# Performance work log

Measured on AMD Instinct MI355X. Metric: run time of the kernel, lower is better.

The kernel has to match this reference:

```python
import jax, jax.numpy as jnp
from jax import lax
import numpy as np

DN = ('NCHW', 'OIHW', 'NCHW')

def conv(x, w, b, stride=1, groups=1):
    y = lax.conv_general_dilated(x, w, (stride, stride), 'SAME',
                                 feature_group_count=groups, dimension_numbers=DN)
    return y + b[None, :, None, None]

def sep_conv(x, dw, pw, pb):
    # depthwise 3x3 -> pointwise 1x1 -> ReLU (BN is frozen at identity)
    y = lax.conv_general_dilated(x, dw, (1, 1), 'SAME',
                                 feature_group_count=x.shape[1], dimension_numbers=DN)
    return jax.nn.relu(conv(y, pw, pb))

def up2(x):
    return jnp.repeat(jnp.repeat(x, 2, axis=2), 2, axis=3)

def down2(x):
    return lax.reduce_window(x, -jnp.inf, lax.max, (1, 1, 2, 2), (1, 1, 2, 2), 'VALID')

def fuse(w, *xs):
    # fast normalized fusion
    w = jax.nn.relu(w)
    w = w / (jnp.sum(w) + 1e-4)
    out = w[0] * xs[0]
    for i in range(1, len(xs)):
        out = out + w[i] * xs[i]
    return out

def bifpn_layer(ps, dw, pw, pb, fw2, fw3):
    p3, p4, p5, p6, p7 = ps
    p6t = sep_conv(fuse(fw2[0], p6, up2(p7)),  dw[0], pw[0], pb[0])
    p5t = sep_conv(fuse(fw2[1], p5, up2(p6t)), dw[1], pw[1], pb[1])
    p4t = sep_conv(fuse(fw2[2], p4, up2(p5t)), dw[2], pw[2], pb[2])
    p3o = sep_conv(fuse(fw2[3], p3, up2(p4t)), dw[3], pw[3], pb[3])
    p4o = sep_conv(fuse(fw3[0], p4, p4t, down2(p3o)), dw[4], pw[4], pb[4])
    p5o = sep_conv(fuse(fw3[1], p5, p5t, down2(p4o)), dw[5], pw[5], pb[5])
    p6o = sep_conv(fuse(fw3[2], p6, p6t, down2(p5o)), dw[6], pw[6], pb[6])
    p7o = sep_conv(fuse(fw2[4], p7, down2(p6o)),      dw[7], pw[7], pb[7])
    return [p3o, p4o, p5o, p6o, p7o]

def make_anchors(img_size):
    # RetinaNet-style anchors: pyramid levels 3..7, 3 scales x 3 ratios
    ratios = np.array([0.5, 1.0, 2.0])
    scales = 2.0 ** (np.arange(3) / 3.0)
    boxes_all = []
    for lvl in range(3, 8):
        stride = 2 ** lvl
        size = 2 ** (lvl + 2)
        fs = img_size // stride
        ws = (size * scales[None, :] / np.sqrt(ratios)[:, None]).reshape(-1)  # [9]
        hs = (size * scales[None, :] * np.sqrt(ratios)[:, None]).reshape(-1)
        ctr = (np.arange(fs) + 0.5) * stride
        gy, gx = np.meshgrid(ctr, ctr, indexing='ij')
        centers = np.stack([gx, gy], -1).reshape(-1, 1, 2)      # [HW,1,2] (x,y)
        wh = np.stack([ws, hs], -1)[None]                       # [1,9,2]
        boxes = np.concatenate([centers - wh / 2, centers + wh / 2], -1).reshape(-1, 4)
        boxes_all.append(boxes)
    return jnp.asarray(np.concatenate(boxes_all, 0), jnp.float32)

def run_head(p, tw, tb, ow, ob, out_ch):
    x = p
    for i in range(tw.shape[0]):
        x = jax.nn.relu(conv(x, tw[i], tb[i]))
    y = conv(x, ow, ob)                                  # [B, 9*out_ch, H, W]
    B, _, H, W = y.shape
    return y.transpose(0, 2, 3, 1).reshape(B, H * W * 9, out_ch)

def setup_inputs() -> dict:
    key = jax.random.key(0)
    ks = iter(jax.random.split(key, 64))
    B, W, NC, ST, D = 4, 88, 90, 3, 4
    chans = [40, 80, 112, 192, 320]
    hw = [64, 32, 16, 8, 4]
    inp = {}
    for i, (c, h) in enumerate(zip(chans, hw)):
        inp[f'c{i+3}'] = jax.random.normal(next(ks), (B, c, h, h), jnp.float32)
        inp[f'lat_w{i+3}'] = jax.random.normal(next(ks), (W, c, 1, 1), jnp.float32) * 0.05
        inp[f'lat_b{i+3}'] = jnp.zeros((W,), jnp.float32)
    inp['bif_dw'] = jax.random.normal(next(ks), (ST, 8, W, 1, 3, 3), jnp.float32) * 0.1
    inp['bif_pw'] = jax.random.normal(next(ks), (ST, 8, W, W, 1, 1), jnp.float32) * 0.05
    inp['bif_pb'] = jnp.zeros((ST, 8, W), jnp.float32)
    inp['bif_fw2'] = jnp.ones((ST, 5, 2), jnp.float32)
    inp['bif_fw3'] = jnp.ones((ST, 3, 3), jnp.float32)
    inp['reg_tw'] = jax.random.normal(next(ks), (D, W, W, 3, 3), jnp.float32) * 0.03
    inp['reg_tb'] = jnp.zeros((D, W), jnp.float32)
    inp['reg_ow'] = jax.random.normal(next(ks), (36, W, 3, 3), jnp.float32) * 0.01
    inp['reg_ob'] = jnp.zeros((36,), jnp.float32)
    inp['cls_tw'] = jax.random.normal(next(ks), (D, W, W, 3, 3), jnp.float32) * 0.03
    inp['cls_tb'] = jnp.zeros((D, W), jnp.float32)
    inp['cls_ow'] = jax.random.normal(next(ks), (9 * NC, W, 3, 3), jnp.float32) * 0.01
    inp['cls_ob'] = jnp.full((9 * NC,), -np.log((1.0 - 0.01) / 0.01), jnp.float32)
    inp['img_size'] = 512
    return inp

def reference(c3, c4, c5, c6, c7,
              lat_w3, lat_b3, lat_w4, lat_b4, lat_w5, lat_b5,
              lat_w6, lat_b6, lat_w7, lat_b7,
              bif_dw, bif_pw, bif_pb, bif_fw2, bif_fw3,
              reg_tw, reg_tb, reg_ow, reg_ob,
              cls_tw, cls_tb, cls_ow, cls_ob,
              img_size):
    num_classes = cls_ow.shape[0] // 9
    ps = [conv(c3, lat_w3, lat_b3), conv(c4, lat_w4, lat_b4), conv(c5, lat_w5, lat_b5),
          conv(c6, lat_w6, lat_b6), conv(c7, lat_w7, lat_b7)]
    for s in range(bif_dw.shape[0]):
        ps = bifpn_layer(ps, bif_dw[s], bif_pw[s], bif_pb[s], bif_fw2[s], bif_fw3[s])
    regression = jnp.concatenate([run_head(p, reg_tw, reg_tb, reg_ow, reg_ob, 4) for p in ps], axis=1)
    classification = jnp.concatenate(
        [jax.nn.sigmoid(run_head(p, cls_tw, cls_tb, cls_ow, cls_ob, num_classes)) for p in ps], axis=1)
    anchors = make_anchors(int(img_size))
    return classification, regression, anchors
```

## Files before the change

kernel.cpp:

```cpp
#include <hip/hip_runtime.h>
#include <math.h>

#define TPB 256
static inline int cdiv(int a, int b) { return (a + b - 1) / b; }

typedef __attribute__((ext_vector_type(8))) short short8;
typedef __attribute__((ext_vector_type(4))) float floatx4;

__device__ __forceinline__ float bf2f(ushort u) {
    union { unsigned int u; float f; } v; v.u = ((unsigned int)u) << 16; return v.f;
}
__device__ __forceinline__ ushort f2bf(float f) {
    union { float f; unsigned int u; } v; v.f = f;
    unsigned int r = (v.u + 0x7FFFu + ((v.u >> 16) & 1u)) >> 16;
    return (ushort)r;
}

#define CONC_ROWS 21824
__device__ __forceinline__ void lvl_of(int row, int& lvl, int& base) {
    lvl = 0; base = 0;
    if (row >= 16384) { lvl = 1; base = 16384; }
    if (row >= 20480) { lvl = 2; base = 20480; }
    if (row >= 21504) { lvl = 3; base = 21504; }
    if (row >= 21760) { lvl = 4; base = 21760; }
}
__constant__ int LOFFc[5] = {0, 36864, 46080, 48384, 48960};

__global__ void pack3_k(const float* __restrict__ w, ushort* __restrict__ Bp,
                        int Ntot, int CO, int total) {
    int idx = blockIdx.x * blockDim.x + threadIdx.x;
    if (idx >= total) return;
    int j = idx & 7; int t = idx >> 3;
    int n = t % Ntot; t /= Ntot;
    int g = t & 3; t >>= 2;
    int ks = t % 3; int tap = t / 3;
    int ci = ks * 32 + g * 8 + j;
    float v = (ci < 88 && n < CO) ? w[((size_t)n * 88 + ci) * 9 + tap] : 0.f;
    Bp[idx] = f2bf(v);
}

__global__ void pack_tw8_k(const float* __restrict__ rw, const float* __restrict__ cw,
                           ushort* __restrict__ Bp) {
    int idx = blockIdx.x * blockDim.x + threadIdx.x;
    if (idx >= 8 * 82944) return;
    int i = idx / 82944; int r = idx - i * 82944;
    const float* w = (i < 4) ? rw + (size_t)i * 69696 : cw + (size_t)(i - 4) * 69696;
    int j = r & 7; int t = r >> 3;
    int n = t % 96; t /= 96;
    int g = t & 3; t >>= 2;
    int ks = t % 3; int tap = t / 3;
    int ci = ks * 32 + g * 8 + j;
    float v = (ci < 88 && n < 88) ? w[((size_t)n * 88 + ci) * 9 + tap] : 0.f;
    Bp[idx] = f2bf(v);
}

__global__ void pack_pw_all_k(const float* __restrict__ pw, ushort* __restrict__ Bp,
                              int total) {
    int idx = blockIdx.x * blockDim.x + threadIdx.x;
    if (idx >= total) return;
    int cid = idx / 9216; int r = idx - cid * 9216;
    int j = r & 7; int t = r >> 3;
    int n = t % 96; t /= 96;
    int g = t & 3; int ks = t >> 2;
    int ci = ks * 32 + g * 8 + j;
    float v = (ci < 88 && n < 88) ? pw[(size_t)cid * 7744 + n * 88 + ci] : 0.f;
    Bp[idx] = f2bf(v);
}

__global__ void pack_lat_k(const float* __restrict__ w3, const float* __restrict__ w4,
                           const float* __restrict__ w5, const float* __restrict__ w6,
                           const float* __restrict__ w7, ushort* __restrict__ Bp) {
    int idx = blockIdx.x * blockDim.x + threadIdx.x;
    if (idx >= 76800) return;
    int l, off;
    if (idx < 6144)       { l = 0; off = 0; }
    else if (idx < 15360) { l = 1; off = 6144; }
    else if (idx < 27648) { l = 2; off = 15360; }
    else if (idx < 46080) { l = 3; off = 27648; }
    else                  { l = 4; off = 46080; }
    const float* w = l == 0 ? w3 : l == 1 ? w4 : l == 2 ? w5 : l == 3 ? w6 : w7;
    const int cins[5] = {40, 80, 112, 192, 320};
    int Cin = cins[l];
    int r = idx - off;
    int j = r & 7; int t = r >> 3;
    int n = t % 96; t /= 96;
    int g = t & 3; int ks = t >> 2;
    int ci = ks * 32 + g * 8 + j;
    float v = (ci < Cin && n < 88) ? w[(size_t)n * Cin + ci] : 0.f;
    Bp[idx] = f2bf(v);
}

__global__ __launch_bounds__(256)
void lateral_mfma_k(const float* __restrict__ x, const ushort* __restrict__ Bp,
                    const float* __restrict__ bias, ushort* __restrict__ out,
                    int Cin, int KS, int logHH) {
    __shared__ ushort As[64 * 40];
    int tid = threadIdx.x;
    int m0 = blockIdx.x * 64;
    int lane = tid & 63, l15 = lane & 15, g = (lane >> 4) & 3;
    int wave = tid >> 6, wm = wave & 1, wn = wave >> 1;
    floatx4 acc[2][3];
#pragma unroll
    for (int a = 0; a < 2; ++a)
#pragma unroll
        for (int b = 0; b < 3; ++b) acc[a][b] = (floatx4){0.f, 0.f, 0.f, 0.f};
    const short8* Bq = (const short8*)Bp;

    int p = m0 + lane;
    int n = p >> logHH, pp = p & ((1 << logHH) - 1);
    const float* xp = x + (((size_t)n * Cin) << logHH) + pp;

    for (int ks = 0; ks < KS; ++ks) {
        __syncthreads();
#pragma unroll
        for (int it = 0; it < 8; ++it) {
            int ciL = (tid >> 6) + it * 4;
            int ci = ks * 32 + ciL;
            float v = (ci < Cin) ? xp[(size_t)ci << logHH] : 0.f;
            As[lane * 40 + ciL] = f2bf(v);
        }
        __syncthreads();
        short8 a0 = *(const short8*)(&As[(wm * 32 + l15) * 40 + g * 8]);
        short8 a1 = *(const short8*)(&As[(wm * 32 + 16 + l15) * 40 + g * 8]);
        int bbase = (ks * 4 + g) * 96 + wn * 48 + l15;
#pragma unroll
        for (int nf = 0; nf < 3; ++nf) {
            short8 b = Bq[bbase + nf * 16];
            acc[0][nf] = __builtin_amdgcn_mfma_f32_16x16x32_bf16(a0, b, acc[0][nf], 0, 0, 0);
            acc[1][nf] = __builtin_amdgcn_mfma_f32_16x16x32_bf16(a1, b, acc[1][nf], 0, 0, 0);
        }
    }
    float bc[3];
#pragma unroll
    for (int nf = 0; nf < 3; ++nf) {
        int c = wn * 48 + nf * 16 + l15;
        bc[nf] = (c < 88) ? bias[c] : 0.f;
    }
#pragma unroll
    for (int mf = 0; mf < 2; ++mf)
#pragma unroll
        for (int r = 0; r < 4; ++r) {
            int pl = m0 + wm * 32 + mf * 16 + g * 4 + r;
#pragma unroll
            for (int nf = 0; nf < 3; ++nf) {
                int c = wn * 48 + nf * 16 + l15;
                out[(size_t)pl * 96 + c] = f2bf(acc[mf][nf][r] + bc[nf]);
            }
        }
}

template <int MODE>
__global__ void fusedw_k(const ushort* __restrict__ a, const ushort* __restrict__ b,
                         const ushort* __restrict__ cmap, const float* __restrict__ fw,
                         const float* __restrict__ dww, ushort* __restrict__ out,
                         int logH, int total) {
    int idx = blockIdx.x * blockDim.x + threadIdx.x;
    if (idx >= total) return;
    int c = idx % 96, p = idx / 96;
    if (c >= 88) { out[idx] = 0; return; }
    int H = 1 << logH;
    int HH = H * H;
    int n = p >> (2 * logH), pp = p & (HH - 1);
    int y = pp >> logH, x = pp & (H - 1);
    float w0 = fmaxf(fw[0], 0.f), w1 = fmaxf(fw[1], 0.f);
    float w2 = (MODE == 2) ? fmaxf(fw[2], 0.f) : 0.f;
    float inv = 1.f / (w0 + w1 + w2 + 1e-4f);
    const float* wp = dww + c * 9;
    float acc = 0.f;
#pragma unroll
    for (int ky = 0; ky < 3; ++ky) {
        int sy = y + ky - 1;
        if (sy < 0 || sy >= H) continue;
#pragma unroll
        for (int kx = 0; kx < 3; ++kx) {
            int sx = x + kx - 1;
            if (sx < 0 || sx >= H) continue;
            int np = n * HH + sy * H + sx;
            float av = bf2f(a[(size_t)np * 96 + c]);
            float fv;
            if (MODE == 0) {
                int Hh = H >> 1;
                int bp = n * Hh * Hh + (sy >> 1) * Hh + (sx >> 1);
                fv = (w0 * av + w1 * bf2f(b[(size_t)bp * 96 + c])) * inv;
            } else {
                int H2 = H * 2;
                const ushort* q = (MODE == 1 ? b : cmap) +
                    ((size_t)(n * H2 * H2 + 2 * sy * H2 + 2 * sx)) * 96 + c;
                float m = fmaxf(fmaxf(bf2f(q[0]), bf2f(q[96])),
                                fmaxf(bf2f(q[H2 * 96]), bf2f(q[H2 * 96 + 96])));
                if (MODE == 1) fv = (w0 * av + w1 * m) * inv;
                else {
                    float b2v = bf2f(b[(size_t)np * 96 + c]);
                    fv = (w0 * av + w1 * b2v + w2 * m) * inv;
                }
            }
            acc = fmaf(fv, wp[ky * 3 + kx], acc);
        }
    }
    out[idx] = f2bf(acc);
}

__global__ __launch_bounds__(256)
void pw_mfma_k(const ushort* __restrict__ in, const ushort* __restrict__ Bp,
               const float* __restrict__ bias, ushort* __restrict__ out) {
    __shared__ ushort As[64 * 104];
    int tid = threadIdx.x;
    int m0 = blockIdx.x * 64;
    int lane = tid & 63, l15 = lane & 15, g = (lane >> 4) & 3;
    int wave = tid >> 6, wm = wave & 1, wn = wave >> 1;
    floatx4 acc[2][3];
#pragma unroll
    for (int a = 0; a < 2; ++a)
#pragma unroll
        for (int b = 0; b < 3; ++b) acc[a][b] = (floatx4){0.f, 0.f, 0.f, 0.f};
    const short8* Bq = (const short8*)Bp;
#pragma unroll
    for (int it = 0; it < 3; ++it) {
        int cc = tid + it * 256;
        int row = cc / 12, cg = cc - row * 12;
        *(uint4*)(&As[row * 104 + cg * 8]) =
            *(const uint4*)(in + (size_t)(m0 + row) * 96 + cg * 8);
    }
    __syncthreads();
#pragma unroll
    for (int ks = 0; ks < 3; ++ks) {
        int k = ks * 32 + g * 8;
        short8 a0 = *(const short8*)(&As[(wm * 32 + l15) * 104 + k]);
        short8 a1 = *(const short8*)(&As[(wm * 32 + 16 + l15) * 104 + k]);
        int bbase = (ks * 4 + g) * 96 + wn * 48 + l15;
#pragma unroll
        for (int nf = 0; nf < 3; ++nf) {
            short8 b = Bq[bbase + nf * 16];
            acc[0][nf] = __builtin_amdgcn_mfma_f32_16x16x32_bf16(a0, b, acc[0][nf], 0, 0, 0);
            acc[1][nf] = __builtin_amdgcn_mfma_f32_16x16x32_bf16(a1, b, acc[1][nf], 0, 0, 0);
        }
    }
    float bc[3];
#pragma unroll
    for (int nf = 0; nf < 3; ++nf) {
        int c = wn * 48 + nf * 16 + l15;
        bc[nf] = (c < 88) ? bias[c] : 0.f;
    }
#pragma unroll
    for (int mf = 0; mf < 2; ++mf)
#pragma unroll
        for (int r = 0; r < 4; ++r) {
            int pl = m0 + wm * 32 + mf * 16 + g * 4 + r;
#pragma unroll
            for (int nf = 0; nf < 3; ++nf) {
                int c = wn * 48 + nf * 16 + l15;
                out[(size_t)pl * 96 + c] = f2bf(fmaxf(acc[mf][nf][r] + bc[nf], 0.f));
            }
        }
}

__global__ __launch_bounds__(256)
void tower_mfma_k(const ushort* __restrict__ inR, const ushort* __restrict__ inC,
                  const ushort* __restrict__ BpR, const ushort* __restrict__ BpC,
                  const float* __restrict__ bR, const float* __restrict__ bC,
                  ushort* __restrict__ outR, ushort* __restrict__ outC) {
    int head = blockIdx.y;
    const ushort* in = head ? inC : inR;
    const ushort* Bp = head ? BpC : BpR;
    const float* bias = head ? bC : bR;
    ushort* out = head ? outC : outR;

    __shared__ ushort As[64 * 104];
    int tid = threadIdx.x;
    int m0 = blockIdx.x * 64;
    int lvl, base; lvl_of(m0, lvl, base);
    int logW = 6 - lvl, W = 1 << logW, HH = W * W, log2HH = 2 * logW;
    int pl0 = m0 - base;
    int lane = tid & 63, l15 = lane & 15, g = (lane >> 4) & 3;
    int wave = tid >> 6, wm = wave & 1, wn = wave >> 1;
    floatx4 acc[2][3];
#pragma unroll
    for (int a = 0; a < 2; ++a)
#pragma unroll
        for (int b = 0; b < 3; ++b) acc[a][b] = (floatx4){0.f, 0.f, 0.f, 0.f};
    const short8* Bq = (const short8*)Bp;

#pragma unroll
    for (int tap = 0; tap < 9; ++tap) {
        int dy = tap / 3 - 1, dx = tap % 3 - 1;
        __syncthreads();
#pragma unroll
        for (int it = 0; it < 3; ++it) {
            int cc = tid + it * 256;
            int row = cc / 12, cg = cc - row * 12;
            int pl = pl0 + row;
            int n = pl >> log2HH, pp = pl & (HH - 1);
            int y = pp >> logW, x = pp & (W - 1);
            int sy = y + dy, sx = x + dx;
            uint4 v = {0u, 0u, 0u, 0u};
            if (sy >= 0 && sy < W && sx >= 0 && sx < W)
                v = *(const uint4*)(in + ((size_t)(base + (n << log2HH) + (sy << logW) + sx)) * 96 + cg * 8);
            *(uint4*)(&As[row * 104 + cg * 8]) = v;
        }
        __syncthreads();
#pragma unroll
        for (int ks = 0; ks < 3; ++ks) {
            int k = ks * 32 + g * 8;
            short8 a0 = *(const short8*)(&As[(wm * 32 + l15) * 104 + k]);
            short8 a1 = *(const short8*)(&As[(wm * 32 + 16 + l15) * 104 + k]);
            int bbase = ((tap * 3 + ks) * 4 + g) * 96 + wn * 48 + l15;
#pragma unroll
            for (int nf = 0; nf < 3; ++nf) {
                short8 b = Bq[bbase + nf * 16];
                acc[0][nf] = __builtin_amdgcn_mfma_f32_16x16x32_bf16(a0, b, acc[0][nf], 0, 0, 0);
                acc[1][nf] = __builtin_amdgcn_mfma_f32_16x16x32_bf16(a1, b, acc[1][nf], 0, 0, 0);
            }
        }
    }
    float bc[3];
#pragma unroll
    for (int nf = 0; nf < 3; ++nf) {
        int c = wn * 48 + nf * 16 + l15;
        bc[nf] = (c < 88) ? bias[c] : 0.f;
    }
#pragma unroll
    for (int mf = 0; mf < 2; ++mf)
#pragma unroll
        for (int r = 0; r < 4; ++r) {
            int pl = m0 + wm * 32 + mf * 16 + g * 4 + r;
#pragma unroll
            for (int nf = 0; nf < 3; ++nf) {
                int c = wn * 48 + nf * 16 + l15;
                out[(size_t)pl * 96 + c] = f2bf(fmaxf(acc[mf][nf][r] + bc[nf], 0.f));
            }
        }
}

template <bool SIG>
__global__ __launch_bounds__(256)
void head_out_all_k(const ushort* __restrict__ in, const ushort* __restrict__ Bp,
                    const float* __restrict__ bias, float* __restrict__ outb,
                    int Ntot, int C9, int OC) {
    __shared__ ushort As[64 * 104];
    int tid = threadIdx.x;
    int m0 = blockIdx.x * 64;
    int n0b = blockIdx.y * 96;
    int lvl, base; lvl_of(m0, lvl, base);
    int logW = 6 - lvl, W = 1 << logW, HH = W * W, log2HH = 2 * logW;
    int pl0 = m0 - base;
    int lane = tid & 63, l15 = lane & 15, g = (lane >> 4) & 3;
    int wave = tid >> 6, wm = wave & 1, wn = wave >> 1;
    floatx4 acc[2][3];
#pragma unroll
    for (int a = 0; a < 2; ++a)
#pragma unroll
        for (int b = 0; b < 3; ++b) acc[a][b] = (floatx4){0.f, 0.f, 0.f, 0.f};
    const short8* Bq = (const short8*)Bp;

    for (int tap = 0; tap < 9; ++tap) {
        int dy = tap / 3 - 1, dx = tap % 3 - 1;
        __syncthreads();
#pragma unroll
        for (int it = 0; it < 3; ++it) {
            int cc = tid + it * 256;
            int row = cc / 12, cg = cc - row * 12;
            int pl = pl0 + row;
            int n = pl >> log2HH, pp = pl & (HH - 1);
            int y = pp >> logW, x = pp & (W - 1);
            int sy = y + dy, sx = x + dx;
            uint4 v = {0u, 0u, 0u, 0u};
            if (sy >= 0 && sy < W && sx >= 0 && sx < W)
                v = *(const uint4*)(in + ((size_t)(base + (n << log2HH) + (sy << logW) + sx)) * 96 + cg * 8);
            *(uint4*)(&As[row * 104 + cg * 8]) = v;
        }
        __syncthreads();
#pragma unroll
        for (int ks = 0; ks < 3; ++ks) {
            int k = ks * 32 + g * 8;
            short8 a0 = *(const short8*)(&As[(wm * 32 + l15) * 104 + k]);
            short8 a1 = *(const short8*)(&As[(wm * 32 + 16 + l15) * 104 + k]);
            int bbase = ((tap * 3 + ks) * 4 + g) * Ntot + n0b + wn * 48 + l15;
#pragma unroll
            for (int nf = 0; nf < 3; ++nf) {
                short8 b = Bq[bbase + nf * 16];
                acc[0][nf] = __builtin_amdgcn_mfma_f32_16x16x32_bf16(a0, b, acc[0][nf], 0, 0, 0);
                acc[1][nf] = __builtin_amdgcn_mfma_f32_16x16x32_bf16(a1, b, acc[1][nf], 0, 0, 0);
            }
        }
    }
#pragma unroll
    for (int nf = 0; nf < 3; ++nf) {
        int c = n0b + wn * 48 + nf * 16 + l15;
        if (c >= C9) continue;
        float bcv = bias[c];
        int a = c / OC, kk = c - a * OC;
#pragma unroll
        for (int mf = 0; mf < 2; ++mf)
#pragma unroll
            for (int r = 0; r < 4; ++r) {
                int pl = pl0 + wm * 32 + mf * 16 + g * 4 + r;
                int n = pl >> log2HH, pp = pl & (HH - 1);
                float v = acc[mf][nf][r] + bcv;
                if (SIG) v = 1.f / (1.f + expf(-v));
                outb[((size_t)n * 49104 + LOFFc[lvl] + (size_t)pp * 9 + a) * OC + kk] = v;
            }
    }
}

__global__ void anchors_k(float* __restrict__ out) {
    int idx = blockIdx.x * blockDim.x + threadIdx.x;
    if (idx >= 49104) return;
    const int offs[6] = {0, 36864, 46080, 48384, 48960, 49104};
    int l = 0;
    while (idx >= offs[l + 1]) ++l;
    int j = idx - offs[l];
    int a = j % 9;
    int p = j / 9;
    int fs = 64 >> l;
    int stride = 8 << l;
    float size = (float)(32 << l);
    int ix = p % fs, iy = p / fs;
    float cx = (ix + 0.5f) * (float)stride;
    float cy = (iy + 0.5f) * (float)stride;
    const float scl[3] = {1.0f, 1.2599210498948732f, 1.5874010519681994f};
    const float sqr[3] = {0.7071067811865476f, 1.0f, 1.4142135623730951f};
    int r = a / 3, s = a % 3;
    float w = size * scl[s] / sqr[r];
    float h = size * scl[s] * sqr[r];
    float* o = out + (size_t)idx * 4;
    o[0] = cx - 0.5f * w;
    o[1] = cy - 0.5f * h;
    o[2] = cx + 0.5f * w;
    o[3] = cy + 0.5f * h;
}


extern "C" void kernel_launch(void* const* d_in, const int* in_sizes, int n_in,
                              void* d_out, int out_size, void* d_ws, size_t ws_size,
                              hipStream_t stream) {
    const float* c_in[5]  = {(const float*)d_in[0],  (const float*)d_in[3],
                             (const float*)d_in[6],  (const float*)d_in[9],
                             (const float*)d_in[12]};
    const float* lat_w[5] = {(const float*)d_in[1],  (const float*)d_in[4],
                             (const float*)d_in[7],  (const float*)d_in[10],
                             (const float*)d_in[13]};
    const float* lat_b[5] = {(const float*)d_in[2],  (const float*)d_in[5],
                             (const float*)d_in[8],  (const float*)d_in[11],
                             (const float*)d_in[14]};
    const float* bif_dw  = (const float*)d_in[15];
    const float* bif_pw  = (const float*)d_in[16];
    const float* bif_pb  = (const float*)d_in[17];
    const float* bif_fw2 = (const float*)d_in[18];
    const float* bif_fw3 = (const float*)d_in[19];
    const float* reg_tw  = (const float*)d_in[20];
    const float* reg_tb  = (const float*)d_in[21];
    const float* reg_ow  = (const float*)d_in[22];
    const float* reg_ob  = (const float*)d_in[23];
    const float* cls_tw  = (const float*)d_in[24];
    const float* cls_tb  = (const float*)d_in[25];
    const float* cls_ow  = (const float*)d_in[26];
    const float* cls_ob  = (const float*)d_in[27];

    const int HS[5]   = {64, 32, 16, 8, 4};
    const int CINL[5] = {40, 80, 112, 192, 320};
    const int KSL[5]  = {2, 3, 4, 6, 10};
    const int LATO[5] = {0, 6144, 15360, 27648, 46080};
    const int ROFF[5] = {0, 16384, 20480, 21504, 21760};
    const int ML[5]   = {16384, 4096, 1024, 256, 64};
    const size_t CONC = (size_t)CONC_ROWS * 96;

    ushort* ws = (ushort*)d_ws;
    size_t off = 0;
    ushort* CA = ws + off; off += CONC;
    ushort* CB = ws + off; off += CONC;
    ushort* T4 = ws + off; off += (size_t)4096 * 96;
    ushort* T5 = ws + off; off += (size_t)1024 * 96;
    ushort* T6 = ws + off; off += (size_t)256 * 96;
    ushort* DT = ws + off; off += (size_t)16384 * 96;
    ushort* HXR0 = ws + off; off += CONC;
    ushort* HXR1 = ws + off; off += CONC;
    ushort* HXC0 = ws + off; off += CONC;
    ushort* HXC1 = ws + off; off += CONC;
    ushort* BP_PW  = ws + off; off += (size_t)24 * 9216;
    ushort* BP_TW  = ws + off; off += (size_t)8 * 82944;
    ushort* BP_RO  = ws + off; off += (size_t)82944;
    ushort* BP_CO  = ws + off; off += (size_t)746496;
    ushort* BP_LAT = ws + off; off += (size_t)76800;
    (void)ws_size; (void)n_in; (void)in_sizes; (void)out_size;

    pack_pw_all_k<<<cdiv(24 * 9216, TPB), TPB, 0, stream>>>(bif_pw, BP_PW, 24 * 9216);
    pack_tw8_k<<<cdiv(8 * 82944, TPB), TPB, 0, stream>>>(reg_tw, cls_tw, BP_TW);
    pack3_k<<<cdiv(82944, TPB), TPB, 0, stream>>>(reg_ow, BP_RO, 96, 36, 82944);
    pack3_k<<<cdiv(746496, TPB), TPB, 0, stream>>>(cls_ow, BP_CO, 864, 810, 746496);
    pack_lat_k<<<cdiv(76800, TPB), TPB, 0, stream>>>(
        lat_w[0], lat_w[1], lat_w[2], lat_w[3], lat_w[4], BP_LAT);

    float* cls_base = (float*)d_out;
    float* reg_base = cls_base + (size_t)4 * 49104 * 90;
    float* anc_base = reg_base + (size_t)4 * 49104 * 4;
    anchors_k<<<cdiv(49104, TPB), TPB, 0, stream>>>(anc_base);

    for (int l = 0; l < 5; ++l) {
        int logHH = 2 * (6 - l);
        lateral_mfma_k<<<ML[l] / 64, 256, 0, stream>>>(
            c_in[l], BP_LAT + LATO[l], lat_b[l], CA + (size_t)ROFF[l] * 96,
            CINL[l], KSL[l], logHH);
    }

    ushort* cur = CA; ushort* nxt = CB;
    for (int s = 0; s < 3; ++s) {
        const float* dws = bif_dw + (size_t)s * 8 * 792;
        const float* pbs = bif_pb + (size_t)s * 8 * 88;
        const float* f2  = bif_fw2 + (size_t)s * 10;
        const float* f3  = bif_fw3 + (size_t)s * 9;
        auto LP = [&](ushort* buf, int l) { return buf + (size_t)ROFF[l] * 96; };
        auto pw = [&](int ci, const ushort* src, ushort* dst, int l) {
            pw_mfma_k<<<ML[l] / 64, 256, 0, stream>>>(
                src, BP_PW + (size_t)(s * 8 + ci) * 9216, pbs + ci * 88, dst);
        };

        { int l = 3, t = ML[l] * 96;
          fusedw_k<0><<<cdiv(t, TPB), TPB, 0, stream>>>(
              LP(cur, 3), LP(cur, 4), nullptr, f2 + 0, dws + 0 * 792, DT, 6 - l, t);
          pw(0, DT, T6, l); }
        { int l = 2, t = ML[l] * 96;
          fusedw_k<0><<<cdiv(t, TPB), TPB, 0, stream>>>(
              LP(cur, 2), T6, nullptr, f2 + 2, dws + 1 * 792, DT, 6 - l, t);
          pw(1, DT, T5, l); }
        { int l = 1, t = ML[l] * 96;
          fusedw_k<0><<<cdiv(t, TPB), TPB, 0, stream>>>(
              LP(cur, 1), T5, nullptr, f2 + 4, dws + 2 * 792, DT, 6 - l, t);
          pw(2, DT, T4, l); }
        { int l = 0, t = ML[l] * 96;
          fusedw_k<0><<<cdiv(t, TPB), TPB, 0, stream>>>(
              LP(cur, 0), T4, nullptr, f2 + 6, dws + 3 * 792, DT, 6 - l, t);
          pw(3, DT, LP(nxt, 0), l); }
        { int l = 1, t = ML[l] * 96;
          fusedw_k<2><<<cdiv(t, TPB), TPB, 0, stream>>>(
              LP(cur, 1), T4, LP(nxt, 0), f3 + 0, dws + 4 * 792, DT, 6 - l, t);
          pw(4, DT, LP(nxt, 1), l); }
        { int l = 2, t = ML[l] * 96;
          fusedw_k<2><<<cdiv(t, TPB), TPB, 0, stream>>>(
              LP(cur, 2), T5, LP(nxt, 1), f3 + 3, dws + 5 * 792, DT, 6 - l, t);
          pw(5, DT, LP(nxt, 2), l); }
        { int l = 3, t = ML[l] * 96;
          fusedw_k<2><<<cdiv(t, TPB), TPB, 0, stream>>>(
              LP(cur, 3), T6, LP(nxt, 2), f3 + 6, dws + 6 * 792, DT, 6 - l, t);
          pw(6, DT, LP(nxt, 3), l); }
        { int l = 4, t = ML[l] * 96;
          fusedw_k<1><<<cdiv(t, TPB), TPB, 0, stream>>>(
              LP(cur, 4), LP(nxt, 3), nullptr, f2 + 8, dws + 7 * 792, DT, 6 - l, t);
          pw(7, DT, LP(nxt, 4), l); }

        ushort* tp = cur; cur = nxt; nxt = tp;
    }

    ushort* hxr[2] = {HXR0, HXR1};
    ushort* hxc[2] = {HXC0, HXC1};
    const ushort* xr = cur;
    const ushort* xc = cur;
    const int GB = CONC_ROWS / 64;
    for (int i = 0; i < 4; ++i) {
        tower_mfma_k<<<dim3(GB, 2), 256, 0, stream>>>(
            xr, xc, BP_TW + (size_t)i * 82944, BP_TW + (size_t)(4 + i) * 82944,
            reg_tb + i * 88, cls_tb + i * 88, hxr[i & 1], hxc[i & 1]);
        xr = hxr[i & 1]; xc = hxc[i & 1];
    }
    head_out_all_k<false><<<dim3(GB, 1), 256, 0, stream>>>(
        xr, BP_RO, reg_ob, reg_base, 96, 36, 4);
    head_out_all_k<true><<<dim3(GB, 9), 256, 0, stream>>>(
        xc, BP_CO, cls_ob, cls_base, 864, 810, 90);
}
```

Measured before the change: 686.5 us.

## Fuse BiFPN depthwise+pointwise into one kernel and use halo tiles for head convs

```diff
diff --git a/kernel.cpp b/kernel.cpp
--- a/kernel.cpp
+++ b/kernel.cpp
@@ -25,6 +25,7 @@
     if (row >= 21760) { lvl = 4; base = 21760; }
 }
 __constant__ int LOFFc[5] = {0, 36864, 46080, 48384, 48960};
+__constant__ int MLVc[5]  = {16384, 4096, 1024, 256, 64};
 
 __global__ void pack3_k(const float* __restrict__ w, ushort* __restrict__ Bp,
                         int Ntot, int CO, int total) {
@@ -150,83 +151,130 @@
 }
 
 template <int MODE>
-__global__ void fusedw_k(const ushort* __restrict__ a, const ushort* __restrict__ b,
-                         const ushort* __restrict__ cmap, const float* __restrict__ fw,
-                         const float* __restrict__ dww, ushort* __restrict__ out,
-                         int logH, int total) {
-    int idx = blockIdx.x * blockDim.x + threadIdx.x;
-    if (idx >= total) return;
-    int c = idx % 96, p = idx / 96;
-    if (c >= 88) { out[idx] = 0; return; }
-    int H = 1 << logH;
-    int HH = H * H;
-    int n = p >> (2 * logH), pp = p & (HH - 1);
-    int y = pp >> logH, x = pp & (H - 1);
+__global__ __launch_bounds__(256, 2)
+void sepconv_k(const ushort* __restrict__ a, const ushort* __restrict__ bsrc,
+               const ushort* __restrict__ csrc, const float* __restrict__ fw,
+               const float* __restrict__ dww, const ushort* __restrict__ Bp,
+               const float* __restrict__ pbias, ushort* __restrict__ out,
+               int logW) {
+    __shared__ ushort Fs[195 * 104];
+    __shared__ ushort Ds[64 * 104];
+    __shared__ ushort Dwb[108 * 8];
+    int tid = threadIdx.x;
+    int W = 1 << logW, HH = W * W, log2HH = 2 * logW;
+    int Mlv = 4 * HH;
+    int HB = W + 1;
+    int RS = 64 + 2 * HB;
+    int pl0 = blockIdx.x * 64;
     float w0 = fmaxf(fw[0], 0.f), w1 = fmaxf(fw[1], 0.f);
     float w2 = (MODE == 2) ? fmaxf(fw[2], 0.f) : 0.f;
     float inv = 1.f / (w0 + w1 + w2 + 1e-4f);
-    const float* wp = dww + c * 9;
-    float acc = 0.f;
-#pragma unroll
-    for (int ky = 0; ky < 3; ++ky) {
-        int sy = y + ky - 1;
-        if (sy < 0 || sy >= H) continue;
-#pragma unroll
-        for (int kx = 0; kx < 3; ++kx) {
-            int sx = x + kx - 1;
-            if (sx < 0 || sx >= H) continue;
-            int np = n * HH + sy * H + sx;
-            float av = bf2f(a[(size_t)np * 96 + c]);
-            float fv;
+    float w0i = w0 * inv, w1i = w1 * inv, w2i = w2 * inv;
+
+    if (tid < 13) *(uint4*)(&Fs[194 * 104 + tid * 8]) = (uint4){0u, 0u, 0u, 0u};
+    for (int i = tid; i < 108; i += 256) {
+        int cg = i / 9, tap = i - cg * 9;
+        ushort tmp[8];
+#pragma unroll
+        for (int j = 0; j < 8; ++j) {
+            int c = cg * 8 + j;
+            tmp[j] = (c < 88) ? f2bf(dww[c * 9 + tap]) : (ushort)0;
+        }
+        *(uint4*)(&Dwb[i * 8]) = *(uint4*)tmp;
+    }
+    for (int i = tid; i < RS * 12; i += 256) {
+        int row = i / 12, cg = i - row * 12;
+        int pl = pl0 - HB + row;
+        uint4 res = {0u, 0u, 0u, 0u};
+        if (pl >= 0 && pl < Mlv) {
+            int n = pl >> log2HH, pp = pl & (HH - 1);
+            int y = pp >> logW, x = pp & (W - 1);
+            uint4 av = *(const uint4*)(a + (size_t)pl * 96 + cg * 8);
+            const ushort* au = (const ushort*)&av;
+            float f[8];
             if (MODE == 0) {
-                int Hh = H >> 1;
-                int bp = n * Hh * Hh + (sy >> 1) * Hh + (sx >> 1);
-                fv = (w0 * av + w1 * bf2f(b[(size_t)bp * 96 + c])) * inv;
+                int Wh = W >> 1;
+                int bp = (n << (log2HH - 2)) + (y >> 1) * Wh + (x >> 1);
+                uint4 bv = *(const uint4*)(bsrc + (size_t)bp * 96 + cg * 8);
+                const ushort* bu = (const ushort*)&bv;
+#pragma unroll
+                for (int j = 0; j < 8; ++j)
+                    f[j] = w0i * bf2f(au[j]) + w1i * bf2f(bu[j]);
             } else {
-                int H2 = H * 2;
-                const ushort* q = (MODE == 1 ? b : cmap) +
-                    ((size_t)(n * H2 * H2 + 2 * sy * H2 + 2 * sx)) * 96 + c;
-                float m = fmaxf(fmaxf(bf2f(q[0]), bf2f(q[96])),
-                                fmaxf(bf2f(q[H2 * 96]), bf2f(q[H2 * 96 + 96])));
-                if (MODE == 1) fv = (w0 * av + w1 * m) * inv;
-                else {
-                    float b2v = bf2f(b[(size_t)np * 96 + c]);
-                    fv = (w0 * av + w1 * b2v + w2 * m) * inv;
+                int W2 = W << 1;
+                const ushort* q = (MODE == 1 ? bsrc : csrc) +
+                    ((size_t)((n << (log2HH + 2)) + (2 * y) * W2 + 2 * x)) * 96 + cg * 8;
+                uint4 q0 = *(const uint4*)(q);
+                uint4 q1 = *(const uint4*)(q + 96);
+                uint4 q2 = *(const uint4*)(q + (size_t)W2 * 96);
+                uint4 q3 = *(const uint4*)(q + (size_t)W2 * 96 + 96);
+                const ushort* u0 = (const ushort*)&q0; const ushort* u1 = (const ushort*)&q1;
+                const ushort* u2 = (const ushort*)&q2; const ushort* u3 = (const ushort*)&q3;
+                if (MODE == 1) {
+#pragma unroll
+                    for (int j = 0; j < 8; ++j) {
+                        float m = fmaxf(fmaxf(bf2f(u0[j]), bf2f(u1[j])),
+                                        fmaxf(bf2f(u2[j]), bf2f(u3[j])));
+                        f[j] = w0i * bf2f(au[j]) + w1i * m;
+                    }
+                } else {
+                    uint4 b2v = *(const uint4*)(bsrc + (size_t)pl * 96 + cg * 8);
+                    const ushort* b2u = (const ushort*)&b2v;
+#pragma unroll
+                    for (int j = 0; j < 8; ++j) {
+                        float m = fmaxf(fmaxf(bf2f(u0[j]), bf2f(u1[j])),
+                                        fmaxf(bf2f(u2[j]), bf2f(u3[j])));
+                        f[j] = w0i * bf2f(au[j]) + w1i * bf2f(b2u[j]) + w2i * m;
+                    }
                 }
             }
-            acc = fmaf(fv, wp[ky * 3 + kx], acc);
-        }
-    }
-    out[idx] = f2bf(acc);
-}
-
-__global__ __launch_bounds__(256)
-void pw_mfma_k(const ushort* __restrict__ in, const ushort* __restrict__ Bp,
-               const float* __restrict__ bias, ushort* __restrict__ out) {
-    __shared__ ushort As[64 * 104];
-    int tid = threadIdx.x;
-    int m0 = blockIdx.x * 64;
+            ushort tmp[8];
+#pragma unroll
+            for (int j = 0; j < 8; ++j) tmp[j] = f2bf(f[j]);
+            res = *(uint4*)tmp;
+        }
+        *(uint4*)(&Fs[row * 104 + cg * 8]) = res;
+    }
+    __syncthreads();
+    for (int i = tid; i < 768; i += 256) {
+        int row = i / 12, cg = i - row * 12;
+        int pl = pl0 + row;
+        int pp = pl & (HH - 1);
+        int y = pp >> logW, x = pp & (W - 1);
+        float acc8[8] = {0.f, 0.f, 0.f, 0.f, 0.f, 0.f, 0.f, 0.f};
+        if (cg < 11) {
+#pragma unroll
+            for (int tap = 0; tap < 9; ++tap) {
+                int dy = tap / 3 - 1, dx = tap % 3 - 1;
+                int sy = y + dy, sx = x + dx;
+                bool pred = ((unsigned)sy < (unsigned)W) && ((unsigned)sx < (unsigned)W);
+                int rsel = pred ? (row + HB + dy * W + dx) : 194;
+                short8 fv = *(const short8*)(&Fs[rsel * 104 + cg * 8]);
+                short8 wv = *(const short8*)(&Dwb[(cg * 9 + tap) * 8]);
+#pragma unroll
+                for (int j = 0; j < 8; ++j)
+                    acc8[j] = fmaf(bf2f((ushort)fv[j]), bf2f((ushort)wv[j]), acc8[j]);
+            }
+        }
+        ushort tmp[8];
+#pragma unroll
+        for (int j = 0; j < 8; ++j) tmp[j] = f2bf(acc8[j]);
+        *(uint4*)(&Ds[row * 104 + cg * 8]) = *(uint4*)tmp;
+    }
+    __syncthreads();
     int lane = tid & 63, l15 = lane & 15, g = (lane >> 4) & 3;
     int wave = tid >> 6, wm = wave & 1, wn = wave >> 1;
     floatx4 acc[2][3];
 #pragma unroll
-    for (int a = 0; a < 2; ++a)
-#pragma unroll
-        for (int b = 0; b < 3; ++b) acc[a][b] = (floatx4){0.f, 0.f, 0.f, 0.f};
+    for (int aa = 0; aa < 2; ++aa)
+#pragma unroll
+        for (int bb = 0; bb < 3; ++bb) acc[aa][bb] = (floatx4){0.f, 0.f, 0.f, 0.f};
     const short8* Bq = (const short8*)Bp;
-#pragma unroll
-    for (int it = 0; it < 3; ++it) {
-        int cc = tid + it * 256;
-        int row = cc / 12, cg = cc - row * 12;
-        *(uint4*)(&As[row * 104 + cg * 8]) =
-            *(const uint4*)(in + (size_t)(m0 + row) * 96 + cg * 8);
-    }
-    __syncthreads();
 #pragma unroll
     for (int ks = 0; ks < 3; ++ks) {
         int k = ks * 32 + g * 8;
-        short8 a0 = *(const short8*)(&As[(wm * 32 + l15) * 104 + k]);
-        short8 a1 = *(const short8*)(&As[(wm * 32 + 16 + l15) * 104 + k]);
+        short8 a0 = *(const short8*)(&Ds[(wm * 32 + l15) * 104 + k]);
+        short8 a1 = *(const short8*)(&Ds[(wm * 32 + 16 + l15) * 104 + k]);
         int bbase = (ks * 4 + g) * 96 + wn * 48 + l15;
 #pragma unroll
         for (int nf = 0; nf < 3; ++nf) {
@@ -239,13 +287,13 @@
 #pragma unroll
     for (int nf = 0; nf < 3; ++nf) {
         int c = wn * 48 + nf * 16 + l15;
-        bc[nf] = (c < 88) ? bias[c] : 0.f;
+        bc[nf] = (c < 88) ? pbias[c] : 0.f;
     }
 #pragma unroll
     for (int mf = 0; mf < 2; ++mf)
 #pragma unroll
         for (int r = 0; r < 4; ++r) {
-            int pl = m0 + wm * 32 + mf * 16 + g * 4 + r;
+            int pl = pl0 + wm * 32 + mf * 16 + g * 4 + r;
 #pragma unroll
             for (int nf = 0; nf < 3; ++nf) {
                 int c = wn * 48 + nf * 16 + l15;
@@ -254,61 +302,73 @@
         }
 }
 
-__global__ __launch_bounds__(256)
-void tower_mfma_k(const ushort* __restrict__ inR, const ushort* __restrict__ inC,
+__global__ __launch_bounds__(256, 2)
+void tower_halo_k(const ushort* __restrict__ inR, const ushort* __restrict__ inC,
                   const ushort* __restrict__ BpR, const ushort* __restrict__ BpC,
                   const float* __restrict__ bR, const float* __restrict__ bC,
                   ushort* __restrict__ outR, ushort* __restrict__ outC) {
+    __shared__ ushort As[259 * 104];
     int head = blockIdx.y;
     const ushort* in = head ? inC : inR;
-    const ushort* Bp = head ? BpC : BpR;
+    const short8* Bq = (const short8*)(head ? BpC : BpR);
     const float* bias = head ? bC : bR;
     ushort* out = head ? outC : outR;
-
-    __shared__ ushort As[64 * 104];
     int tid = threadIdx.x;
-    int m0 = blockIdx.x * 64;
+    int m0 = blockIdx.x * 128;
     int lvl, base; lvl_of(m0, lvl, base);
     int logW = 6 - lvl, W = 1 << logW, HH = W * W, log2HH = 2 * logW;
-    int pl0 = m0 - base;
+    int Mlv = MLVc[lvl];
+    int HB = W + 1;
+    int RS = 128 + 2 * HB;
+    if (tid < 13) *(uint4*)(&As[258 * 104 + tid * 8]) = (uint4){0u, 0u, 0u, 0u};
+    for (int i = tid; i < RS * 12; i += 256) {
+        int row = i / 12, cg = i - row * 12;
+        int pl = m0 - base - HB + row;
+        uint4 v = {0u, 0u, 0u, 0u};
+        if (pl >= 0 && pl < Mlv)
+            v = *(const uint4*)(in + (size_t)(base + pl) * 96 + cg * 8);
+        *(uint4*)(&As[row * 104 + cg * 8]) = v;
+    }
+    __syncthreads();
     int lane = tid & 63, l15 = lane & 15, g = (lane >> 4) & 3;
     int wave = tid >> 6, wm = wave & 1, wn = wave >> 1;
-    floatx4 acc[2][3];
-#pragma unroll
-    for (int a = 0; a < 2; ++a)
-#pragma unroll
-        for (int b = 0; b < 3; ++b) acc[a][b] = (floatx4){0.f, 0.f, 0.f, 0.f};
-    const short8* Bq = (const short8*)Bp;
-
+    int pl0 = m0 - base;
+    int rL[4], xm[4], ym[4]; bool vm[4];
+#pragma unroll
+    for (int mf = 0; mf < 4; ++mf) {
+        rL[mf] = wm * 64 + mf * 16 + l15;
+        int pl = pl0 + rL[mf];
+        vm[mf] = pl < Mlv;
+        int pp = pl & (HH - 1);
+        ym[mf] = pp >> logW; xm[mf] = pp & (W - 1);
+    }
+    floatx4 acc[4][3];
+#pragma unroll
+    for (int aa = 0; aa < 4; ++aa)
+#pragma unroll
+        for (int bb = 0; bb < 3; ++bb) acc[aa][bb] = (floatx4){0.f, 0.f, 0.f, 0.f};
 #pragma unroll
     for (int tap = 0; tap < 9; ++tap) {
         int dy = tap / 3 - 1, dx = tap % 3 - 1;
-        __syncthreads();
-#pragma unroll
-        for (int it = 0; it < 3; ++it) {
-            int cc = tid + it * 256;
-            int row = cc / 12, cg = cc - row * 12;
-            int pl = pl0 + row;
-            int n = pl >> log2HH, pp = pl & (HH - 1);
-            int y = pp >> logW, x = pp & (W - 1);
-            int sy = y + dy, sx = x + dx;
-            uint4 v = {0u, 0u, 0u, 0u};
-            if (sy >= 0 && sy < W && sx >= 0 && sx < W)
-                v = *(const uint4*)(in + ((size_t)(base + (n << log2HH) + (sy << logW) + sx)) * 96 + cg * 8);
-            *(uint4*)(&As[row * 104 + cg * 8]) = v;
-        }
-        __syncthreads();
+        int rs[4];
+#pragma unroll
+        for (int mf = 0; mf < 4; ++mf) {
+            bool pred = vm[mf] && ((unsigned)(ym[mf] + dy) < (unsigned)W) &&
+                        ((unsigned)(xm[mf] + dx) < (unsigned)W);
+            rs[mf] = pred ? (HB + rL[mf] + dy * W + dx) : 258;
+        }
 #pragma unroll
         for (int ks = 0; ks < 3; ++ks) {
-            int k = ks * 32 + g * 8;
-            short8 a0 = *(const short8*)(&As[(wm * 32 + l15) * 104 + k]);
-            short8 a1 = *(const short8*)(&As[(wm * 32 + 16 + l15) * 104 + k]);
+            short8 bfr[3];
             int bbase = ((tap * 3 + ks) * 4 + g) * 96 + wn * 48 + l15;
 #pragma unroll
-            for (int nf = 0; nf < 3; ++nf) {
-                short8 b = Bq[bbase + nf * 16];
-                acc[0][nf] = __builtin_amdgcn_mfma_f32_16x16x32_bf16(a0, b, acc[0][nf], 0, 0, 0);
-                acc[1][nf] = __builtin_amdgcn_mfma_f32_16x16x32_bf16(a1, b, acc[1][nf], 0, 0, 0);
+            for (int nf = 0; nf < 3; ++nf) bfr[nf] = Bq[bbase + nf * 16];
+#pragma unroll
+            for (int mf = 0; mf < 4; ++mf) {
+                short8 af = *(const short8*)(&As[rs[mf] * 104 + ks * 32 + g * 8]);
+#pragma unroll
+                for (int nf = 0; nf < 3; ++nf)
+                    acc[mf][nf] = __builtin_amdgcn_mfma_f32_16x16x32_bf16(af, bfr[nf], acc[mf][nf], 0, 0, 0);
             }
         }
     }
@@ -319,67 +379,83 @@
         bc[nf] = (c < 88) ? bias[c] : 0.f;
     }
 #pragma unroll
-    for (int mf = 0; mf < 2; ++mf)
+    for (int mf = 0; mf < 4; ++mf)
 #pragma unroll
         for (int r = 0; r < 4; ++r) {
-            int pl = m0 + wm * 32 + mf * 16 + g * 4 + r;
+            int pl = pl0 + wm * 64 + mf * 16 + g * 4 + r;
+            if (pl >= Mlv) continue;
 #pragma unroll
             for (int nf = 0; nf < 3; ++nf) {
                 int c = wn * 48 + nf * 16 + l15;
-                out[(size_t)pl * 96 + c] = f2bf(fmaxf(acc[mf][nf][r] + bc[nf], 0.f));
-            }
-        }
-}
-
-template <bool SIG>
-__global__ __launch_bounds__(256)
-void head_out_all_k(const ushort* __restrict__ in, const ushort* __restrict__ Bp,
-                    const float* __restrict__ bias, float* __restrict__ outb,
-                    int Ntot, int C9, int OC) {
-    __shared__ ushort As[64 * 104];
+                out[(size_t)(base + pl) * 96 + c] = f2bf(fmaxf(acc[mf][nf][r] + bc[nf], 0.f));
+            }
+        }
+}
+
+template <int OC, bool SIG>
+__global__ __launch_bounds__(256, 2)
+void head_halo_k(const ushort* __restrict__ in, const ushort* __restrict__ Bp,
+                 const float* __restrict__ bias, float* __restrict__ outb,
+                 int Ntot, int C9) {
+    __shared__ ushort As[259 * 104];
     int tid = threadIdx.x;
-    int m0 = blockIdx.x * 64;
+    int m0 = blockIdx.x * 128;
     int n0b = blockIdx.y * 96;
     int lvl, base; lvl_of(m0, lvl, base);
     int logW = 6 - lvl, W = 1 << logW, HH = W * W, log2HH = 2 * logW;
-    int pl0 = m0 - base;
+    int Mlv = MLVc[lvl];
+    int HB = W + 1;
+    int RS = 128 + 2 * HB;
+    if (tid < 13) *(uint4*)(&As[258 * 104 + tid * 8]) = (uint4){0u, 0u, 0u, 0u};
+    for (int i = tid; i < RS * 12; i += 256) {
+        int row = i / 12, cg = i - row * 12;
+        int pl = m0 - base - HB + row;
+        uint4 v = {0u, 0u, 0u, 0u};
+        if (pl >= 0 && pl < Mlv)
+            v = *(const uint4*)(in + (size_t)(base + pl) * 96 + cg * 8);
+        *(uint4*)(&As[row * 104 + cg * 8]) = v;
+    }
+    __syncthreads();
     int lane = tid & 63, l15 = lane & 15, g = (lane >> 4) & 3;
     int wave = tid >> 6, wm = wave & 1, wn = wave >> 1;
-    floatx4 acc[2][3];
-#pragma unroll
-    for (int a = 0; a < 2; ++a)
-#pragma unroll
-        for (int b = 0; b < 3; ++b) acc[a][b] = (floatx4){0.f, 0.f, 0.f, 0.f};
+    int pl0 = m0 - base;
+    int rL[4], xm[4], ym[4]; bool vm[4];
+#pragma unroll
+    for (int mf = 0; mf < 4; ++mf) {
+        rL[mf] = wm * 64 + mf * 16 + l15;
+        int pl = pl0 + rL[mf];
+        vm[mf] = pl < Mlv;
+        int pp = pl & (HH - 1);
+        ym[mf] = pp >> logW; xm[mf] = pp & (W - 1);
+    }
+    floatx4 acc[4][3];
+#pragma unroll
+    for (int aa = 0; aa < 4; ++aa)
+#pragma unroll
+        for (int bb = 0; bb < 3; ++bb) acc[aa][bb] = (floatx4){0.f, 0.f, 0.f, 0.f};
     const short8* Bq = (const short8*)Bp;
-
+#pragma unroll
     for (int tap = 0; tap < 9; ++tap) {
         int dy = tap / 3 - 1, dx = tap % 3 - 1;
-        __syncthreads();
-#pragma unroll
-        for (int it = 0; it < 3; ++it) {
-            int cc = tid + it * 256;
-            int row = cc / 12, cg = cc - row * 12;
-            int pl = pl0 + row;
-            int n = pl >> log2HH, pp = pl & (HH - 1);
-            int y = pp >> logW, x = pp & (W - 1);
-            int sy = y + dy, sx = x + dx;
-            uint4 v = {0u, 0u, 0u, 0u};
-            if (sy >= 0 && sy < W && sx >= 0 && sx < W)
-                v = *(const uint4*)(in + ((size_t)(base + (n << log2HH) + (sy << logW) + sx)) * 96 + cg * 8);
-            *(uint4*)(&As[row * 104 + cg * 8]) = v;
-        }
-        __syncthreads();
+        int rs[4];
+#pragma unroll
+        for (int mf = 0; mf < 4; ++mf) {
+            bool pred = vm[mf] && ((unsigned)(ym[mf] + dy) < (unsigned)W) &&
+                        ((unsigned)(xm[mf] + dx) < (unsigned)W);
+            rs[mf] = pred ? (HB + rL[mf] + dy * W + dx) : 258;
+        }
 #pragma unroll
         for (int ks = 0; ks < 3; ++ks) {
-            int k = ks * 32 + g * 8;
-            short8 a0 = *(const short8*)(&As[(wm * 32 + l15) * 104 + k]);
-            short8 a1 = *(const short8*)(&As[(wm * 32 + 16 + l15) * 104 + k]);
+            short8 bfr[3];
             int bbase = ((tap * 3 + ks) * 4 + g) * Ntot + n0b + wn * 48 + l15;
 #pragma unroll
-            for (int nf = 0; nf < 3; ++nf) {
-                short8 b = Bq[bbase + nf * 16];
-                acc[0][nf] = __builtin_amdgcn_mfma_f32_16x16x32_bf16(a0, b, acc[0][nf], 0, 0, 0);
-                acc[1][nf] = __builtin_amdgcn_mfma_f32_16x16x32_bf16(a1, b, acc[1][nf], 0, 0, 0);
+            for (int nf = 0; nf < 3; ++nf) bfr[nf] = Bq[bbase + nf * 16];
+#pragma unroll
+            for (int mf = 0; mf < 4; ++mf) {
+                short8 af = *(const short8*)(&As[rs[mf] * 104 + ks * 32 + g * 8]);
+#pragma unroll
+                for (int nf = 0; nf < 3; ++nf)
+                    acc[mf][nf] = __builtin_amdgcn_mfma_f32_16x16x32_bf16(af, bfr[nf], acc[mf][nf], 0, 0, 0);
             }
         }
     }
@@ -390,10 +466,11 @@
         float bcv = bias[c];
         int a = c / OC, kk = c - a * OC;
 #pragma unroll
-        for (int mf = 0; mf < 2; ++mf)
+        for (int mf = 0; mf < 4; ++mf)
 #pragma unroll
             for (int r = 0; r < 4; ++r) {
-                int pl = pl0 + wm * 32 + mf * 16 + g * 4 + r;
+                int pl = pl0 + wm * 64 + mf * 16 + g * 4 + r;
+                if (pl >= Mlv) continue;
                 int n = pl >> log2HH, pp = pl & (HH - 1);
                 float v = acc[mf][nf][r] + bcv;
                 if (SIG) v = 1.f / (1.f + expf(-v));
@@ -456,7 +533,6 @@
     const float* cls_ow  = (const float*)d_in[26];
     const float* cls_ob  = (const float*)d_in[27];
 
-    const int HS[5]   = {64, 32, 16, 8, 4};
     const int CINL[5] = {40, 80, 112, 192, 320};
     const int KSL[5]  = {2, 3, 4, 6, 10};
     const int LATO[5] = {0, 6144, 15360, 27648, 46080};
@@ -471,7 +547,6 @@
     ushort* T4 = ws + off; off += (size_t)4096 * 96;
     ushort* T5 = ws + off; off += (size_t)1024 * 96;
     ushort* T6 = ws + off; off += (size_t)256 * 96;
-    ushort* DT = ws + off; off += (size_t)16384 * 96;
     ushort* HXR0 = ws + off; off += CONC;
     ushort* HXR1 = ws + off; off += CONC;
     ushort* HXC0 = ws + off; off += CONC;
@@ -509,60 +584,41 @@
         const float* f2  = bif_fw2 + (size_t)s * 10;
         const float* f3  = bif_fw3 + (size_t)s * 9;
         auto LP = [&](ushort* buf, int l) { return buf + (size_t)ROFF[l] * 96; };
-        auto pw = [&](int ci, const ushort* src, ushort* dst, int l) {
-            pw_mfma_k<<<ML[l] / 64, 256, 0, stream>>>(
-                src, BP_PW + (size_t)(s * 8 + ci) * 9216, pbs + ci * 88, dst);
-        };
-
-        { int l = 3, t = ML[l] * 96;
-          fusedw_k<0><<<cdiv(t, TPB), TPB, 0, stream>>>(
-              LP(cur, 3), LP(cur, 4), nullptr, f2 + 0, dws + 0 * 792, DT, 6 - l, t);
-          pw(0, DT, T6, l); }
-        { int l = 2, t = ML[l] * 96;
-          fusedw_k<0><<<cdiv(t, TPB), TPB, 0, stream>>>(
-              LP(cur, 2), T6, nullptr, f2 + 2, dws + 1 * 792, DT, 6 - l, t);
-          pw(1, DT, T5, l); }
-        { int l = 1, t = ML[l] * 96;
-          fusedw_k<0><<<cdiv(t, TPB), TPB, 0, stream>>>(
-              LP(cur, 1), T5, nullptr, f2 + 4, dws + 2 * 792, DT, 6 - l, t);
-          pw(2, DT, T4, l); }
-        { int l = 0, t = ML[l] * 96;
-          fusedw_k<0><<<cdiv(t, TPB), TPB, 0, stream>>>(
-              LP(cur, 0), T4, nullptr, f2 + 6, dws + 3 * 792, DT, 6 - l, t);
-          pw(3, DT, LP(nxt, 0), l); }
-        { int l = 1, t = ML[l] * 96;
-          fusedw_k<2><<<cdiv(t, TPB), TPB, 0, stream>>>(
-              LP(cur, 1), T4, LP(nxt, 0), f3 + 0, dws + 4 * 792, DT, 6 - l, t);
-          pw(4, DT, LP(nxt, 1), l); }
-        { int l = 2, t = ML[l] * 96;
-          fusedw_k<2><<<cdiv(t, TPB), TPB, 0, stream>>>(
-              LP(cur, 2), T5, LP(nxt, 1), f3 + 3, dws + 5 * 792, DT, 6 - l, t);
-          pw(5, DT, LP(nxt, 2), l); }
-        { int l = 3, t = ML[l] * 96;
-          fusedw_k<2><<<cdiv(t, TPB), TPB, 0, stream>>>(
-              LP(cur, 3), T6, LP(nxt, 2), f3 + 6, dws + 6 * 792, DT, 6 - l, t);
-          pw(6, DT, LP(nxt, 3), l); }
-        { int l = 4, t = ML[l] * 96;
-          fusedw_k<1><<<cdiv(t, TPB), TPB, 0, stream>>>(
-              LP(cur, 4), LP(nxt, 3), nullptr, f2 + 8, dws + 7 * 792, DT, 6 - l, t);
-          pw(7, DT, LP(nxt, 4), l); }
+        auto BPW = [&](int ci) { return BP_PW + (size_t)(s * 8 + ci) * 9216; };
+
+        sepconv_k<0><<<ML[3] / 64, 256, 0, stream>>>(
+            LP(cur, 3), LP(cur, 4), nullptr, f2 + 0, dws + 0 * 792, BPW(0), pbs + 0 * 88, T6, 3);
+        sepconv_k<0><<<ML[2] / 64, 256, 0, stream>>>(
+            LP(cur, 2), T6, nullptr, f2 + 2, dws + 1 * 792, BPW(1), pbs + 1 * 88, T5, 4);
+        sepconv_k<0><<<ML[1] / 64, 256, 0, stream>>>(
+            LP(cur, 1), T5, nullptr, f2 + 4, dws + 2 * 792, BPW(2), pbs + 2 * 88, T4, 5);
+        sepconv_k<0><<<ML[0] / 64, 256, 0, stream>>>(
+            LP(cur, 0), T4, nullptr, f2 + 6, dws + 3 * 792, BPW(3), pbs + 3 * 88, LP(nxt, 0), 6);
+        sepconv_k<2><<<ML[1] / 64, 256, 0, stream>>>(
+            LP(cur, 1), T4, LP(nxt, 0), f3 + 0, dws + 4 * 792, BPW(4), pbs + 4 * 88, LP(nxt, 1), 5);
+        sepconv_k<2><<<ML[2] / 64, 256, 0, stream>>>(
+            LP(cur, 2), T5, LP(nxt, 1), f3 + 3, dws + 5 * 792, BPW(5), pbs + 5 * 88, LP(nxt, 2), 4);
+        sepconv_k<2><<<ML[3] / 64, 256, 0, stream>>>(
+            LP(cur, 3), T6, LP(nxt, 2), f3 + 6, dws + 6 * 792, BPW(6), pbs + 6 * 88, LP(nxt, 3), 3);
+        sepconv_k<1><<<ML[4] / 64, 256, 0, stream>>>(
+            LP(cur, 4), LP(nxt, 3), nullptr, f2 + 8, dws + 7 * 792, BPW(7), pbs + 7 * 88, LP(nxt, 4), 2);
 
         ushort* tp = cur; cur = nxt; nxt = tp;
     }
 
+    const int GB = 171;
     ushort* hxr[2] = {HXR0, HXR1};
     ushort* hxc[2] = {HXC0, HXC1};
     const ushort* xr = cur;
     const ushort* xc = cur;
-    const int GB = CONC_ROWS / 64;
     for (int i = 0; i < 4; ++i) {
-        tower_mfma_k<<<dim3(GB, 2), 256, 0, stream>>>(
+        tower_halo_k<<<dim3(GB, 2), 256, 0, stream>>>(
             xr, xc, BP_TW + (size_t)i * 82944, BP_TW + (size_t)(4 + i) * 82944,
             reg_tb + i * 88, cls_tb + i * 88, hxr[i & 1], hxc[i & 1]);
         xr = hxr[i & 1]; xc = hxc[i & 1];
     }
-    head_out_all_k<false><<<dim3(GB, 1), 256, 0, stream>>>(
-        xr, BP_RO, reg_ob, reg_base, 96, 36, 4);
-    head_out_all_k<true><<<dim3(GB, 9), 256, 0, stream>>>(
-        xc, BP_CO, cls_ob, cls_base, 864, 810, 90);
-}
+    head_halo_k<4, false><<<dim3(GB, 1), 256, 0, stream>>>(
+        xr, BP_RO, reg_ob, reg_base, 96, 36);
+    head_halo_k<90, true><<<dim3(GB, 9), 256, 0, stream>>>(
+        xc, BP_CO, cls_ob, cls_base, 864, 810);
+}
```

Measured after the change: 726.7 us. 1.06x slower.
